# Kernel optimization log

Hardware: AMD Instinct MI355X
Metric: run time of the kernel (lower is better)

Reference implementation:

```python
import jax, jax.numpy as jnp
import numpy as np

OUT, IN, G, TOK = 4096, 4096, 16, 8192


def setup_inputs() -> dict:
    key = jax.random.key(0)
    k1, k2, k3, k4 = jax.random.split(key, 4)
    x = jax.random.normal(k1, (TOK, IN), dtype=jnp.float32)
    # packed int4 pairs: each byte holds two 4-bit values (low nibble, high nibble)
    weight_q4 = jax.random.randint(k2, (OUT * IN // G, G // 2), 0, 256, dtype=jnp.int32)
    # per-group abs-max normalization, strictly positive
    weight_norm = jax.random.uniform(k3, (OUT * IN // G, 1), dtype=jnp.float16, minval=0.01, maxval=1.0)
    bias = jax.random.normal(k4, (OUT,), dtype=jnp.float32) * 0.01
    return {"x": x, "weight_q4": weight_q4, "weight_norm": weight_norm, "bias": bias}


def _dequant_4bit(weight_q4, weight_norm):
    # unpack nibbles: even positions = low nibble, odd positions = high nibble
    low = weight_q4 & 15
    high = (weight_q4 >> 4) & 15
    q8 = jnp.stack([low, high], axis=-1).reshape(weight_q4.shape[0], -1)  # [n_groups, G]
    norm = weight_norm.astype(jnp.float32)                                 # [n_groups, 1]
    w = (q8.astype(jnp.float32) / 15.0) * 2.0 * norm - norm               # [-norm, +norm]
    return w.reshape(OUT, IN)


def reference(x, weight_q4, weight_norm, bias):
    W = _dequant_4bit(weight_q4, weight_norm)  # [OUT, IN] fp32
    return x @ W.T + bias                      # [TOK, OUT]
```

## Files before the change

kernel.cpp:

```cpp
#include <hip/hip_runtime.h>
#include <hip/hip_fp16.h>

#define M_TOK 8192
#define N_OUT 4096
#define K_IN  4096
#define GRP   16

typedef __bf16 bf16x8 __attribute__((ext_vector_type(8)));
typedef float  f32x4  __attribute__((ext_vector_type(4)));
typedef unsigned short ushort8 __attribute__((ext_vector_type(8)));

__device__ __forceinline__ float bfbits(unsigned short h) {
    unsigned int u = ((unsigned int)h) << 16;
    return __builtin_bit_cast(float, u);
}

#define GLDS16(gp, sp) __builtin_amdgcn_global_load_lds(                      \
        (const __attribute__((address_space(1))) void*)(gp),                  \
        (__attribute__((address_space(3))) void*)(sp), 16, 0, 0)

__global__ void detect_modes(const void* __restrict__ xv,
                             const void* __restrict__ nrmv,
                             const void* __restrict__ biasv,
                             int* __restrict__ modes) {
    if (threadIdx.x != 0 || blockIdx.x != 0) return;
    int xm = 1;
    const unsigned short* px = (const unsigned short*)xv;
    for (int i = 0; i < 128; i += 2) {
        unsigned short h = px[i];
        int e = (h >> 7) & 0xFF;
        if (!((e >= 64 && e <= 134) || (h & 0x7FFF) == 0)) { xm = 0; break; }
    }
    const unsigned short* pn = (const unsigned short*)nrmv;
    bool ok16 = true, okbf = true;
    for (int i = 0; i < 32; ++i) {
        unsigned short h = pn[i];
        float v16 = __half2float(__builtin_bit_cast(__half, h));
        float vbf = bfbits(h);
        if (!(v16 > 0.0085f && v16 < 1.02f)) ok16 = false;
        if (!(vbf > 0.0085f && vbf < 1.02f)) okbf = false;
    }
    int bm = 1;
    const unsigned short* pb = (const unsigned short*)biasv;
    for (int i = 0; i < 128; i += 2) {
        unsigned short h = pb[i];
        int e = (h >> 7) & 0xFF;
        if (!((e >= 64 && e <= 134) || (h & 0x7FFF) == 0)) { bm = 0; break; }
    }
    modes[0] = xm;
    modes[1] = ok16 ? 0 : (okbf ? 1 : 2);
    modes[2] = bm;
}

__global__ __launch_bounds__(256) void prep_w(const int* __restrict__ q4,
                                              const void* __restrict__ nrmv,
                                              const int* __restrict__ modes,
                                              __bf16* __restrict__ W) {
    const int nmode = modes[1];
    const int t = blockIdx.x * 256 + threadIdx.x;
    const int4* qp = (const int4*)q4 + (size_t)t * 2;
    int4 a4 = qp[0], c4 = qp[1];
    float nm;
    if (nmode == 0)      nm = __half2float(((const __half*)nrmv)[t]);
    else if (nmode == 1) nm = bfbits(((const unsigned short*)nrmv)[t]);
    else                 nm = ((const float*)nrmv)[t];
    float s = nm * (2.0f / 15.0f);
    int qs[8] = {a4.x, a4.y, a4.z, a4.w, c4.x, c4.y, c4.z, c4.w};
    bf16x8 v0, v1;
#pragma unroll
    for (int u = 0; u < 8; ++u) {
        float lo = fmaf((float)(qs[u] & 15), s, -nm);
        float hi = fmaf((float)((qs[u] >> 4) & 15), s, -nm);
        if (u < 4) { v0[2 * u] = (__bf16)lo; v0[2 * u + 1] = (__bf16)hi; }
        else       { v1[2 * (u - 4)] = (__bf16)lo; v1[2 * (u - 4) + 1] = (__bf16)hi; }
    }
    bf16x8* wp = (bf16x8*)(W + (size_t)t * 16);
    wp[0] = v0; wp[1] = v1;
}

__global__ __launch_bounds__(256) void prep_x(const void* __restrict__ xv,
                                              const int* __restrict__ modes,
                                              __bf16* __restrict__ X) {
    if (modes[0] == 1) return;
    const int total8 = M_TOK * K_IN / 8;
    const int stride = gridDim.x * 256;
    for (int i = blockIdx.x * 256 + threadIdx.x; i < total8; i += stride) {
        const float4* fp = (const float4*)xv + (size_t)i * 2;
        float4 f0 = fp[0], f1 = fp[1];
        bf16x8 u;
        u[0] = (__bf16)f0.x; u[1] = (__bf16)f0.y; u[2] = (__bf16)f0.z; u[3] = (__bf16)f0.w;
        u[4] = (__bf16)f1.x; u[5] = (__bf16)f1.y; u[6] = (__bf16)f1.z; u[7] = (__bf16)f1.w;
        *(bf16x8*)(X + (size_t)i * 8) = u;
    }
}

__global__ __launch_bounds__(256, 3) void gemm_glds(
        const void* __restrict__ xv, const __bf16* __restrict__ Xws,
        const __bf16* __restrict__ W, const void* __restrict__ biasv,
        const int* __restrict__ modes, float* __restrict__ out) {
    __shared__ __align__(16) __bf16 As[128 * 32];
    __shared__ __align__(16) __bf16 Bs[128 * 32];

    const int xmode = modes[0];
    const int bmode = modes[2];
    const __bf16* A = xmode ? (const __bf16*)xv : Xws;

    const int bid = blockIdx.x;
    const int n0 = (bid & 31) * 128;
    const int m0 = (bid >> 5) * 128;

    const int tid = threadIdx.x;
    const int w  = tid >> 6;
    const int l  = tid & 63;
    const int r  = l & 15;
    const int q  = l >> 4;
    const int wm = (w >> 1) * 64;
    const int wn = (w & 1) * 64;

    const int c0 = w * 2;
    const int lr = l >> 2;
    const int lc = (l & 3) * 8;
    const __bf16* ga0 = A + (size_t)(m0 + c0 * 16 + lr) * K_IN + lc;
    const __bf16* gb0 = W + (size_t)(n0 + c0 * 16 + lr) * K_IN + lc;
    __bf16* la0 = As + c0 * 512;
    __bf16* lb0 = Bs + c0 * 512;

    f32x4 acc[4][4];
#pragma unroll
    for (int j = 0; j < 4; ++j) {
        const int bidx = n0 + wn + j * 16 + r;
        float bv = (bmode == 0) ? ((const float*)biasv)[bidx]
                                : bfbits(((const unsigned short*)biasv)[bidx]);
#pragma unroll
        for (int i = 0; i < 4; ++i) {
            acc[i][j][0] = bv; acc[i][j][1] = bv; acc[i][j][2] = bv; acc[i][j][3] = bv;
        }
    }

    for (int k0 = 0; k0 < K_IN; k0 += 32) {
        __syncthreads();
        GLDS16(ga0 + k0,                      la0);
        GLDS16(ga0 + k0 + (size_t)16 * K_IN,  la0 + 512);
        GLDS16(gb0 + k0,                      lb0);
        GLDS16(gb0 + k0 + (size_t)16 * K_IN,  lb0 + 512);
        __syncthreads();

        bf16x8 af[4], bf[4];
#pragma unroll
        for (int i = 0; i < 4; ++i)
            af[i] = *(const bf16x8*)(As + (wm + i * 16 + r) * 32 + q * 8);
#pragma unroll
        for (int j = 0; j < 4; ++j)
            bf[j] = *(const bf16x8*)(Bs + (wn + j * 16 + r) * 32 + q * 8);

#pragma unroll
        for (int i = 0; i < 4; ++i)
#pragma unroll
            for (int j = 0; j < 4; ++j)
                acc[i][j] = __builtin_amdgcn_mfma_f32_16x16x32_bf16(
                    af[i], bf[j], acc[i][j], 0, 0, 0);
    }

#pragma unroll
    for (int i = 0; i < 4; ++i) {
        const int row = m0 + wm + i * 16 + q * 4;
#pragma unroll
        for (int j = 0; j < 4; ++j) {
            const int col = n0 + wn + j * 16 + r;
            float* p = out + (size_t)row * N_OUT + col;
            p[0 * N_OUT] = acc[i][j][0];
            p[1 * N_OUT] = acc[i][j][1];
            p[2 * N_OUT] = acc[i][j][2];
            p[3 * N_OUT] = acc[i][j][3];
        }
    }
}

__global__ __launch_bounds__(256, 2) void gemm_fused(
        const void* __restrict__ xv,
        const int* __restrict__ q4, const void* __restrict__ nrmv,
        const void* __restrict__ biasv, float* __restrict__ out) {
    __shared__ __align__(16) __bf16 As[128 * 32];
    __shared__ __align__(16) __bf16 Bs[128 * 32];
    __shared__ int s_modes[3];

    const int tid = threadIdx.x;

    if (tid == 0) {
        int xm = 1;
        const unsigned short* px = (const unsigned short*)xv;
        for (int i = 0; i < 128; i += 2) {
            unsigned short h = px[i];
            int e = (h >> 7) & 0xFF;
            if (!((e >= 64 && e <= 134) || (h & 0x7FFF) == 0)) { xm = 0; break; }
        }
        const unsigned short* pn = (const unsigned short*)nrmv;
        bool ok16 = true, okbf = true;
        for (int i = 0; i < 32; ++i) {
            unsigned short h = pn[i];
            float v16 = __half2float(__builtin_bit_cast(__half, h));
            float vbf = bfbits(h);
            if (!(v16 > 0.0085f && v16 < 1.02f)) ok16 = false;
            if (!(vbf > 0.0085f && vbf < 1.02f)) okbf = false;
        }
        int bm = 1;
        const unsigned short* pb = (const unsigned short*)biasv;
        for (int i = 0; i < 128; i += 2) {
            unsigned short h = pb[i];
            int e = (h >> 7) & 0xFF;
            if (!((e >= 64 && e <= 134) || (h & 0x7FFF) == 0)) { bm = 0; break; }
        }
        s_modes[0] = xm;
        s_modes[1] = ok16 ? 0 : (okbf ? 1 : 2);
        s_modes[2] = bm;
    }
    __syncthreads();
    const int xmode = s_modes[0];
    const int nmode = s_modes[1];
    const int bmode = s_modes[2];

    const int bid = blockIdx.x;
    const int n0 = (bid & 31) * 128;
    const int m0 = (bid >> 5) * 128;

    const int w  = tid >> 6;
    const int l  = tid & 63;
    const int r  = l & 15;
    const int q  = l >> 4;
    const int wm = (w >> 1) * 64;
    const int wn = (w & 1) * 64;

    const int arow = tid >> 1;
    const int acol = (tid & 1) * 16;
    const size_t aoff = (size_t)(m0 + arow) * K_IN + acol;

    const int brow = tid >> 1;
    const int bgc  = tid & 1;

    f32x4 acc[4][4];
#pragma unroll
    for (int j = 0; j < 4; ++j) {
        const int bidx = n0 + wn + j * 16 + r;
        float bv = (bmode == 0) ? ((const float*)biasv)[bidx]
                                : bfbits(((const unsigned short*)biasv)[bidx]);
#pragma unroll
        for (int i = 0; i < 4; ++i) {
            acc[i][j][0] = bv; acc[i][j][1] = bv; acc[i][j][2] = bv; acc[i][j][3] = bv;
        }
    }

    for (int k0 = 0; k0 < K_IN; k0 += 32) {
        __syncthreads();
        {
            const int g = (n0 + brow) * (K_IN / GRP) + (k0 >> 4) + bgc;
            const int4* qp = (const int4*)q4 + (size_t)g * 2;
            int4 a4 = qp[0], c4 = qp[1];
            float nm;
            if (nmode == 0)      nm = __half2float(((const __half*)nrmv)[g]);
            else if (nmode == 1) nm = bfbits(((const unsigned short*)nrmv)[g]);
            else                 nm = ((const float*)nrmv)[g];
            float s = nm * (2.0f / 15.0f);
            int qs[8] = {a4.x, a4.y, a4.z, a4.w, c4.x, c4.y, c4.z, c4.w};
            bf16x8 v0, v1;
#pragma unroll
            for (int u = 0; u < 8; ++u) {
                float lo = fmaf((float)(qs[u] & 15), s, -nm);
                float hi = fmaf((float)((qs[u] >> 4) & 15), s, -nm);
                if (u < 4) { v0[2 * u] = (__bf16)lo; v0[2 * u + 1] = (__bf16)hi; }
                else       { v1[2 * (u - 4)] = (__bf16)lo; v1[2 * (u - 4) + 1] = (__bf16)hi; }
            }
            bf16x8* bp = (bf16x8*)(Bs + brow * 32 + bgc * 16);
            bp[0] = v0; bp[1] = v1;
        }

        if (xmode == 0) {
            const float4* ap = (const float4*)((const float*)xv + aoff + k0);
            float4 f0 = ap[0], f1 = ap[1], f2 = ap[2], f3 = ap[3];
            bf16x8 u0, u1;
            u0[0] = (__bf16)f0.x; u0[1] = (__bf16)f0.y; u0[2] = (__bf16)f0.z; u0[3] = (__bf16)f0.w;
            u0[4] = (__bf16)f1.x; u0[5] = (__bf16)f1.y; u0[6] = (__bf16)f1.z; u0[7] = (__bf16)f1.w;
            u1[0] = (__bf16)f2.x; u1[1] = (__bf16)f2.y; u1[2] = (__bf16)f2.z; u1[3] = (__bf16)f2.w;
            u1[4] = (__bf16)f3.x; u1[5] = (__bf16)f3.y; u1[6] = (__bf16)f3.z; u1[7] = (__bf16)f3.w;
            bf16x8* asp = (bf16x8*)(As + arow * 32 + acol);
            asp[0] = u0; asp[1] = u1;
        } else {
            const ushort8* ap = (const ushort8*)((const unsigned short*)xv + aoff + k0);
            ushort8 u0 = ap[0], u1 = ap[1];
            bf16x8* asp = (bf16x8*)(As + arow * 32 + acol);
            asp[0] = __builtin_bit_cast(bf16x8, u0);
            asp[1] = __builtin_bit_cast(bf16x8, u1);
        }

        __syncthreads();

        bf16x8 af[4], bf[4];
#pragma unroll
        for (int i = 0; i < 4; ++i)
            af[i] = *(const bf16x8*)(As + (wm + i * 16 + r) * 32 + q * 8);
#pragma unroll
        for (int j = 0; j < 4; ++j)
            bf[j] = *(const bf16x8*)(Bs + (wn + j * 16 + r) * 32 + q * 8);

#pragma unroll
        for (int i = 0; i < 4; ++i)
#pragma unroll
            for (int j = 0; j < 4; ++j)
                acc[i][j] = __builtin_amdgcn_mfma_f32_16x16x32_bf16(
                    af[i], bf[j], acc[i][j], 0, 0, 0);
    }

#pragma unroll
    for (int i = 0; i < 4; ++i) {
        const int row = m0 + wm + i * 16 + q * 4;
#pragma unroll
        for (int j = 0; j < 4; ++j) {
            const int col = n0 + wn + j * 16 + r;
            float* p = out + (size_t)row * N_OUT + col;
            p[0 * N_OUT] = acc[i][j][0];
            p[1 * N_OUT] = acc[i][j][1];
            p[2 * N_OUT] = acc[i][j][2];
            p[3 * N_OUT] = acc[i][j][3];
        }
    }
}

extern "C" void kernel_launch(void* const* d_in, const int* in_sizes, int n_in,
                              void* d_out, int out_size, void* d_ws, size_t ws_size,
                              hipStream_t stream) {
    const void* x    = d_in[0];
    const int*  q4   = (const int*)d_in[1];
    const void* nrm  = d_in[2];
    const void* bias = d_in[3];
    float*      out  = (float*)d_out;

    const size_t W_OFF = 256;
    const size_t X_OFF = W_OFF + (size_t)N_OUT * K_IN * 2;
    const size_t NEED  = X_OFF + (size_t)M_TOK * K_IN * 2;

    if (ws_size >= NEED) {
        int*    modes = (int*)d_ws;
        __bf16* W     = (__bf16*)((char*)d_ws + W_OFF);
        __bf16* X     = (__bf16*)((char*)d_ws + X_OFF);

        detect_modes<<<1, 64, 0, stream>>>(x, nrm, bias, modes);
        prep_w<<<(N_OUT * K_IN / GRP) / 256, 256, 0, stream>>>(q4, nrm, modes, W);
        prep_x<<<2048, 256, 0, stream>>>(x, modes, X);
        gemm_glds<<<(M_TOK / 128) * (N_OUT / 128), 256, 0, stream>>>(
            x, X, W, bias, modes, out);
    } else {
        gemm_fused<<<(M_TOK / 128) * (N_OUT / 128), 256, 0, stream>>>(
            x, q4, nrm, bias, out);
    }
}
```

Baseline: 562.4 us.

## Merge prep kernels, compute modes per block via ballot, swizzle GEMM block order

```diff
diff --git a/kernel.cpp b/kernel.cpp
--- a/kernel.cpp
+++ b/kernel.cpp
@@ -19,93 +19,101 @@
         (const __attribute__((address_space(1))) void*)(gp),                  \
         (__attribute__((address_space(3))) void*)(sp), 16, 0, 0)
 
-__global__ void detect_modes(const void* __restrict__ xv,
-                             const void* __restrict__ nrmv,
-                             const void* __restrict__ biasv,
-                             int* __restrict__ modes) {
-    if (threadIdx.x != 0 || blockIdx.x != 0) return;
-    int xm = 1;
-    const unsigned short* px = (const unsigned short*)xv;
-    for (int i = 0; i < 128; i += 2) {
-        unsigned short h = px[i];
-        int e = (h >> 7) & 0xFF;
-        if (!((e >= 64 && e <= 134) || (h & 0x7FFF) == 0)) { xm = 0; break; }
-    }
-    const unsigned short* pn = (const unsigned short*)nrmv;
-    bool ok16 = true, okbf = true;
-    for (int i = 0; i < 32; ++i) {
-        unsigned short h = pn[i];
-        float v16 = __half2float(__builtin_bit_cast(__half, h));
-        float vbf = bfbits(h);
-        if (!(v16 > 0.0085f && v16 < 1.02f)) ok16 = false;
-        if (!(vbf > 0.0085f && vbf < 1.02f)) okbf = false;
-    }
-    int bm = 1;
-    const unsigned short* pb = (const unsigned short*)biasv;
-    for (int i = 0; i < 128; i += 2) {
-        unsigned short h = pb[i];
-        int e = (h >> 7) & 0xFF;
-        if (!((e >= 64 && e <= 134) || (h & 0x7FFF) == 0)) { bm = 0; break; }
-    }
-    modes[0] = xm;
-    modes[1] = ok16 ? 0 : (okbf ? 1 : 2);
-    modes[2] = bm;
-}
-
-__global__ __launch_bounds__(256) void prep_w(const int* __restrict__ q4,
-                                              const void* __restrict__ nrmv,
-                                              const int* __restrict__ modes,
-                                              __bf16* __restrict__ W) {
-    const int nmode = modes[1];
-    const int t = blockIdx.x * 256 + threadIdx.x;
-    const int4* qp = (const int4*)q4 + (size_t)t * 2;
-    int4 a4 = qp[0], c4 = qp[1];
-    float nm;
-    if (nmode == 0)      nm = __half2float(((const __half*)nrmv)[t]);
-    else if (nmode == 1) nm = bfbits(((const unsigned short*)nrmv)[t]);
-    else                 nm = ((const float*)nrmv)[t];
-    float s = nm * (2.0f / 15.0f);
-    int qs[8] = {a4.x, a4.y, a4.z, a4.w, c4.x, c4.y, c4.z, c4.w};
-    bf16x8 v0, v1;
-#pragma unroll
-    for (int u = 0; u < 8; ++u) {
-        float lo = fmaf((float)(qs[u] & 15), s, -nm);
-        float hi = fmaf((float)((qs[u] >> 4) & 15), s, -nm);
-        if (u < 4) { v0[2 * u] = (__bf16)lo; v0[2 * u + 1] = (__bf16)hi; }
-        else       { v1[2 * (u - 4)] = (__bf16)lo; v1[2 * (u - 4) + 1] = (__bf16)hi; }
-    }
-    bf16x8* wp = (bf16x8*)(W + (size_t)t * 16);
-    wp[0] = v0; wp[1] = v1;
-}
-
-__global__ __launch_bounds__(256) void prep_x(const void* __restrict__ xv,
-                                              const int* __restrict__ modes,
-                                              __bf16* __restrict__ X) {
-    if (modes[0] == 1) return;
-    const int total8 = M_TOK * K_IN / 8;
-    const int stride = gridDim.x * 256;
-    for (int i = blockIdx.x * 256 + threadIdx.x; i < total8; i += stride) {
-        const float4* fp = (const float4*)xv + (size_t)i * 2;
-        float4 f0 = fp[0], f1 = fp[1];
-        bf16x8 u;
-        u[0] = (__bf16)f0.x; u[1] = (__bf16)f0.y; u[2] = (__bf16)f0.z; u[3] = (__bf16)f0.w;
-        u[4] = (__bf16)f1.x; u[5] = (__bf16)f1.y; u[6] = (__bf16)f1.z; u[7] = (__bf16)f1.w;
-        *(bf16x8*)(X + (size_t)i * 8) = u;
+__device__ __forceinline__ void detect_block(const void* __restrict__ xv,
+                                             const void* __restrict__ nrmv,
+                                             const void* __restrict__ biasv,
+                                             int* s_modes) {
+    const int tid = threadIdx.x;
+    if (tid < 64) {
+        const unsigned short* px = (const unsigned short*)xv;
+        unsigned short hx = px[tid * 2];
+        int ex = (hx >> 7) & 0xFF;
+        bool xok = ((ex >= 64 && ex <= 134) || (hx & 0x7FFF) == 0);
+        unsigned long long xb = __ballot(xok);
+
+        const unsigned short* pn = (const unsigned short*)nrmv;
+        unsigned short hn = pn[tid & 31];
+        float v16 = __half2float(__builtin_bit_cast(__half, hn));
+        float vbf = bfbits(hn);
+        unsigned long long b16 = __ballot(v16 > 0.0085f && v16 < 1.02f);
+        unsigned long long bbf = __ballot(vbf > 0.0085f && vbf < 1.02f);
+
+        const unsigned short* pb = (const unsigned short*)biasv;
+        unsigned short hb = pb[tid * 2];
+        int eb = (hb >> 7) & 0xFF;
+        bool bok = ((eb >= 64 && eb <= 134) || (hb & 0x7FFF) == 0);
+        unsigned long long bb = __ballot(bok);
+
+        if (tid == 0) {
+            s_modes[0] = (xb == ~0ULL) ? 1 : 0;
+            s_modes[1] = (b16 == ~0ULL) ? 0 : ((bbf == ~0ULL) ? 1 : 2);
+            s_modes[2] = (bb == ~0ULL) ? 1 : 0;
+        }
+    }
+    __syncthreads();
+}
+
+__global__ __launch_bounds__(256) void prep_all(const void* __restrict__ xv,
+                                                const int* __restrict__ q4,
+                                                const void* __restrict__ nrmv,
+                                                const void* __restrict__ biasv,
+                                                __bf16* __restrict__ W,
+                                                __bf16* __restrict__ X) {
+    __shared__ int s_modes[3];
+    detect_block(xv, nrmv, biasv, s_modes);
+    const int tid = threadIdx.x;
+
+    if (blockIdx.x < 4096) {
+        const int nmode = s_modes[1];
+        const int t = blockIdx.x * 256 + tid;
+        const int4* qp = (const int4*)q4 + (size_t)t * 2;
+        int4 a4 = qp[0], c4 = qp[1];
+        float nm;
+        if (nmode == 0)      nm = __half2float(((const __half*)nrmv)[t]);
+        else if (nmode == 1) nm = bfbits(((const unsigned short*)nrmv)[t]);
+        else                 nm = ((const float*)nrmv)[t];
+        float s = nm * (2.0f / 15.0f);
+        int qs[8] = {a4.x, a4.y, a4.z, a4.w, c4.x, c4.y, c4.z, c4.w};
+        bf16x8 v0, v1;
+#pragma unroll
+        for (int u = 0; u < 8; ++u) {
+            float lo = fmaf((float)(qs[u] & 15), s, -nm);
+            float hi = fmaf((float)((qs[u] >> 4) & 15), s, -nm);
+            if (u < 4) { v0[2 * u] = (__bf16)lo; v0[2 * u + 1] = (__bf16)hi; }
+            else       { v1[2 * (u - 4)] = (__bf16)lo; v1[2 * (u - 4) + 1] = (__bf16)hi; }
+        }
+        bf16x8* wp = (bf16x8*)(W + (size_t)t * 16);
+        wp[0] = v0; wp[1] = v1;
+    } else {
+        if (s_modes[0] == 1) return;
+        const int bx = blockIdx.x - 4096;
+        const int total8 = M_TOK * K_IN / 8;
+        const int stride = 2048 * 256;
+        for (int i = bx * 256 + tid; i < total8; i += stride) {
+            const float4* fp = (const float4*)xv + (size_t)i * 2;
+            float4 f0 = fp[0], f1 = fp[1];
+            bf16x8 u;
+            u[0] = (__bf16)f0.x; u[1] = (__bf16)f0.y; u[2] = (__bf16)f0.z; u[3] = (__bf16)f0.w;
+            u[4] = (__bf16)f1.x; u[5] = (__bf16)f1.y; u[6] = (__bf16)f1.z; u[7] = (__bf16)f1.w;
+            *(bf16x8*)(X + (size_t)i * 8) = u;
+        }
     }
 }
 
 __global__ __launch_bounds__(256, 3) void gemm_glds(
         const void* __restrict__ xv, const __bf16* __restrict__ Xws,
-        const __bf16* __restrict__ W, const void* __restrict__ biasv,
-        const int* __restrict__ modes, float* __restrict__ out) {
+        const __bf16* __restrict__ W, const void* __restrict__ nrmv,
+        const void* __restrict__ biasv, float* __restrict__ out) {
     __shared__ __align__(16) __bf16 As[128 * 32];
     __shared__ __align__(16) __bf16 Bs[128 * 32];
-
-    const int xmode = modes[0];
-    const int bmode = modes[2];
+    __shared__ int s_modes[3];
+
+    detect_block(xv, nrmv, biasv, s_modes);
+    const int xmode = s_modes[0];
+    const int bmode = s_modes[2];
     const __bf16* A = xmode ? (const __bf16*)xv : Xws;
 
-    const int bid = blockIdx.x;
+    const int bid = ((blockIdx.x & 7) << 8) + (blockIdx.x >> 3);
     const int n0 = (bid & 31) * 128;
     const int m0 = (bid >> 5) * 128;
 
@@ -184,37 +192,8 @@
     __shared__ __align__(16) __bf16 Bs[128 * 32];
     __shared__ int s_modes[3];
 
+    detect_block(xv, nrmv, biasv, s_modes);
     const int tid = threadIdx.x;
-
-    if (tid == 0) {
-        int xm = 1;
-        const unsigned short* px = (const unsigned short*)xv;
-        for (int i = 0; i < 128; i += 2) {
-            unsigned short h = px[i];
-            int e = (h >> 7) & 0xFF;
-            if (!((e >= 64 && e <= 134) || (h & 0x7FFF) == 0)) { xm = 0; break; }
-        }
-        const unsigned short* pn = (const unsigned short*)nrmv;
-        bool ok16 = true, okbf = true;
-        for (int i = 0; i < 32; ++i) {
-            unsigned short h = pn[i];
-            float v16 = __half2float(__builtin_bit_cast(__half, h));
-            float vbf = bfbits(h);
-            if (!(v16 > 0.0085f && v16 < 1.02f)) ok16 = false;
-            if (!(vbf > 0.0085f && vbf < 1.02f)) okbf = false;
-        }
-        int bm = 1;
-        const unsigned short* pb = (const unsigned short*)biasv;
-        for (int i = 0; i < 128; i += 2) {
-            unsigned short h = pb[i];
-            int e = (h >> 7) & 0xFF;
-            if (!((e >= 64 && e <= 134) || (h & 0x7FFF) == 0)) { bm = 0; break; }
-        }
-        s_modes[0] = xm;
-        s_modes[1] = ok16 ? 0 : (okbf ? 1 : 2);
-        s_modes[2] = bm;
-    }
-    __syncthreads();
     const int xmode = s_modes[0];
     const int nmode = s_modes[1];
     const int bmode = s_modes[2];
@@ -333,20 +312,16 @@
     const void* bias = d_in[3];
     float*      out  = (float*)d_out;
 
-    const size_t W_OFF = 256;
-    const size_t X_OFF = W_OFF + (size_t)N_OUT * K_IN * 2;
+    const size_t X_OFF = (size_t)N_OUT * K_IN * 2;
     const size_t NEED  = X_OFF + (size_t)M_TOK * K_IN * 2;
 
     if (ws_size >= NEED) {
-        int*    modes = (int*)d_ws;
-        __bf16* W     = (__bf16*)((char*)d_ws + W_OFF);
-        __bf16* X     = (__bf16*)((char*)d_ws + X_OFF);
-
-        detect_modes<<<1, 64, 0, stream>>>(x, nrm, bias, modes);
-        prep_w<<<(N_OUT * K_IN / GRP) / 256, 256, 0, stream>>>(q4, nrm, modes, W);
-        prep_x<<<2048, 256, 0, stream>>>(x, modes, X);
+        __bf16* W = (__bf16*)d_ws;
+        __bf16* X = (__bf16*)((char*)d_ws + X_OFF);
+
+        prep_all<<<4096 + 2048, 256, 0, stream>>>(x, q4, nrm, bias, W, X);
         gemm_glds<<<(M_TOK / 128) * (N_OUT / 128), 256, 0, stream>>>(
-            x, X, W, bias, modes, out);
+            x, X, W, nrm, bias, out);
     } else {
         gemm_fused<<<(M_TOK / 128) * (N_OUT / 128), 256, 0, stream>>>(
             x, q4, nrm, bias, out);
```

Measured after the change: 582.2 us. 3.5% more time.
